# Performance work log

Hardware: AMD Instinct MI355X
Metric: run time of the kernel (lower is better)

The kernel has to match this reference:

```python
import jax, jax.numpy as jnp
import numpy as np

PATCH = 8      # patch_size
NFREQ = 8      # fourie_freq


def _fourier_feats(nH, nW, F, dtype):
    # Per-patch positional Fourier features: sin/cos of normalized patch-center
    # coords at F dyadic frequencies for both axes -> [nH, nW, 4F].
    iy = (jnp.arange(nH, dtype=jnp.float32) + 0.5) / nH
    ix = (jnp.arange(nW, dtype=jnp.float32) + 0.5) / nW
    freqs = (2.0 ** jnp.arange(F, dtype=jnp.float32)) * jnp.pi
    fy = iy[:, None] * freqs[None, :]  # [nH, F]
    fx = ix[:, None] * freqs[None, :]  # [nW, F]
    feats = jnp.concatenate([
        jnp.broadcast_to(jnp.sin(fy)[:, None, :], (nH, nW, F)),
        jnp.broadcast_to(jnp.cos(fy)[:, None, :], (nH, nW, F)),
        jnp.broadcast_to(jnp.sin(fx)[None, :, :], (nH, nW, F)),
        jnp.broadcast_to(jnp.cos(fx)[None, :, :], (nH, nW, F)),
    ], axis=-1)
    return feats.astype(dtype)


def setup_inputs() -> dict:
    key = jax.random.key(0)
    ks = jax.random.split(key, 5)
    B, C, H, W = 16, 64, 128, 128
    E, OC, P, F = 8, 64, PATCH, NFREQ
    GC = C + 4 * F  # gate_channel = 96
    x = jax.random.normal(ks[0], (B, C, H, W), jnp.float32)
    expert_w = jax.random.normal(ks[1], (E, OC, C, 3, 3), jnp.float32) * 0.05
    expert_b = jax.random.normal(ks[2], (E, OC), jnp.float32) * 0.05
    gate_w = jax.random.normal(ks[3], (E, GC * P * P), jnp.float32) * 0.02
    gate_b = jnp.zeros((E,), jnp.float32)
    return {"x": x, "expert_w": expert_w, "expert_b": expert_b,
            "gate_w": gate_w, "gate_b": gate_b}


def reference(x, expert_w, expert_b, gate_w, gate_b):
    B, C, H, W = x.shape
    E, OC = expert_w.shape[0], expert_w.shape[1]
    P, F = PATCH, NFREQ
    nH, nW = H // P, W // P

    # --- gating: per-patch softmax over experts ---
    # patches: [B, nH, nW, C, P, P] (matches nn.Flatten over (C,P,P))
    patches = x.reshape(B, C, nH, P, nW, P).transpose(0, 2, 4, 1, 3, 5)
    feats = _fourier_feats(nH, nW, F, x.dtype)                       # [nH,nW,4F]
    pos = jnp.broadcast_to(feats[None, :, :, :, None, None],
                           (B, nH, nW, 4 * F, P, P))
    gate_in = jnp.concatenate([patches, pos], axis=3).reshape(B, nH, nW, -1)
    logits = jnp.einsum('bhwf,ef->bhwe', gate_in, gate_w) + gate_b
    gate = jax.nn.softmax(logits, axis=-1)                           # [B,nH,nW,E]

    # --- experts: all E convs fused into a single conv, then gated combine ---
    wk = expert_w.reshape(E * OC, C, 3, 3)
    y = jax.lax.conv_general_dilated(
        x, wk, window_strides=(1, 1), padding='SAME',
        dimension_numbers=('NCHW', 'OIHW', 'NCHW'))
    y = y + expert_b.reshape(E * OC)[None, :, None, None]
    y = jax.nn.relu(y).reshape(B, E, OC, H, W)

    # upsample per-patch gates to pixel resolution: [B,E,H,W]
    g = gate.transpose(0, 3, 1, 2)                                   # [B,E,nH,nW]
    g = jnp.repeat(jnp.repeat(g, P, axis=2), P, axis=3)
    out = jnp.einsum('behw,bechw->bchw', g, y)                       # [B,OC,H,W]
    return out
```

## Files before the change

kernel.cpp:

```cpp
#include <hip/hip_runtime.h>

typedef short v8s __attribute__((ext_vector_type(8)));
typedef float v4f __attribute__((ext_vector_type(4)));

#define NCH    64
#define NHH    128
#define NWW    128
#define NOC    64
#define KSTEPS 18

#define COLS 34
#define SLAB_BYTES (6 * COLS * 128)
#define BBUF_OFF   SLAB_BYTES
#define NBUF 3
#define LDSG_OFF   (SLAB_BYTES + NBUF * 8192)
#define SMEM_BYTES (LDSG_OFF + 128)

#define GW_STRIDE 6144

__device__ __forceinline__ unsigned short f2bf(float f) {
  unsigned int u = __float_as_uint(f);
  u += 0x7FFFu + ((u >> 16) & 1u);
  return (unsigned short)(u >> 16);
}

__global__ void pack_b_kernel(const float* __restrict__ ew,
                              unsigned short* __restrict__ bp) {
  int f = blockIdx.x * 256 + threadIdx.x;
  int j = f & 7;
  int t = f >> 3;
  int lane = t & 63;
  t >>= 6;
  int nt = t & 3;
  t >>= 2;
  int e01 = t & 1;
  int gs = t >> 1;
  int sl = gs % KSTEPS;
  int g = gs / KSTEPS;
  int e = g + 4 * e01;
  int k = sl * 32 + (lane >> 4) * 8 + j;
  int n = nt * 16 + (lane & 15);
  int khw = k >> 6;
  int c = k & 63;
  bp[f] = f2bf(ew[((e * NOC + n) * NCH + c) * 9 + khw]);
}

__global__ __launch_bounds__(512) void gate_kernel(
    const float* __restrict__ x,
    const float* __restrict__ gw,
    const float* __restrict__ gb,
    float* __restrict__ gate_out) {
  __shared__ float xs[16][8][132];
  __shared__ float wsum[8][32];
  __shared__ float lg[16][8];

  const int pid = blockIdx.x;
  const int ph = pid & 15;
  const int b = pid >> 4;
  const int tid = threadIdx.x;
  const int e = tid >> 6;
  const int lane = tid & 63;

  if (tid < 256) {
    int e2 = tid >> 5, j = tid & 31;
    const float* p = gw + e2 * GW_STRIDE + 4096 + j * 64;
    float s = 0.f;
#pragma unroll
    for (int g = 0; g < 16; ++g) {
      float4 v = *(const float4*)(p + g * 4);
      s += v.x + v.y + v.z + v.w;
    }
    wsum[e2][j] = s;
  }

  float acc[16];
#pragma unroll
  for (int pw = 0; pw < 16; ++pw) acc[pw] = 0.f;

  const float* xrow = x + ((size_t)(b * NCH) * NHH + ph * 8) * NWW;

  for (int cc = 0; cc < 4; ++cc) {
    __syncthreads();
    for (int i = tid; i < 4096; i += 512) {
      int c = i >> 8;
      int py = (i >> 5) & 7;
      int w4 = i & 31;
      float4 v = *(const float4*)&xrow[(cc * 16 + c) * (NHH * NWW) + py * NWW + w4 * 4];
      *(float4*)&xs[c][py][w4 * 4] = v;
    }
    __syncthreads();
#pragma unroll
    for (int i = 0; i < 4; ++i) {
      int g = lane + 64 * i;
      int pxg = g & 1;
      int py = (g >> 1) & 7;
      int c = g >> 4;
      const float4 wv = *(const float4*)&gw[e * GW_STRIDE + (cc * 16 + c) * 64 + py * 8 + pxg * 4];
      const float* xp = &xs[c][py][pxg * 4];
#pragma unroll
      for (int pw = 0; pw < 16; ++pw) {
        float4 xv = *(const float4*)(xp + pw * 8);
        acc[pw] += xv.x * wv.x + xv.y * wv.y + xv.z * wv.z + xv.w * wv.w;
      }
    }
  }

#pragma unroll
  for (int pw = 0; pw < 16; ++pw) {
    float v = acc[pw];
#pragma unroll
    for (int off = 32; off > 0; off >>= 1) v += __shfl_xor(v, off, 64);
    if (lane == 0) lg[pw][e] = v;
  }
  __syncthreads();

  if (tid < 16) {
    const int pw = tid;
    const float cy = (ph + 0.5f) / 16.0f;
    const float cx = (pw + 0.5f) / 16.0f;
    float l[8];
#pragma unroll
    for (int ee = 0; ee < 8; ++ee) l[ee] = lg[pw][ee] + gb[ee];
    for (int j = 0; j < 32; ++j) {
      float freq = (float)(1 << (j & 7)) * 3.14159265358979323846f;
      float base = (j < 16) ? cy : cx;
      float a = base * freq;
      float v = ((j >> 3) & 1) ? cosf(a) : sinf(a);
#pragma unroll
      for (int ee = 0; ee < 8; ++ee) l[ee] += v * wsum[ee][j];
    }
    float mx = -1e30f;
#pragma unroll
    for (int ee = 0; ee < 8; ++ee) mx = fmaxf(mx, l[ee]);
    float sum = 0.f;
#pragma unroll
    for (int ee = 0; ee < 8; ++ee) { l[ee] = expf(l[ee] - mx); sum += l[ee]; }
    float inv = 1.0f / sum;
#pragma unroll
    for (int ee = 0; ee < 8; ++ee)
      gate_out[(pid * 16 + pw) * 8 + ee] = l[ee] * inv;
  }
}

__device__ __forceinline__ void load_stage(const unsigned short* __restrict__ bp,
                                           char* smem, int gs, int buf,
                                           int wid, int lane) {
  const char* gsrc = (const char*)bp + gs * 8192 + wid * 2048 + lane * 16;
  char* ldst = smem + BBUF_OFF + buf * 8192 + wid * 2048;
  __builtin_amdgcn_global_load_lds(
      (const __attribute__((address_space(1))) void*)gsrc,
      (__attribute__((address_space(3))) void*)ldst, 16, 0, 0);
  __builtin_amdgcn_global_load_lds(
      (const __attribute__((address_space(1))) void*)(gsrc + 1024),
      (__attribute__((address_space(3))) void*)(ldst + 1024), 16, 0, 0);
}

__global__ __launch_bounds__(256, 2) void moe_conv_kernel(
    const float* __restrict__ x,
    const float* __restrict__ eb,
    const unsigned short* __restrict__ bp,
    const float* __restrict__ gate,
    float* __restrict__ out) {
  __shared__ __align__(16) char smem[SMEM_BYTES];
  unsigned short* bbufs = (unsigned short*)(smem + BBUF_OFF);
  float* ldsg = (float*)(smem + LDSG_OFF);

  const int tid = threadIdx.x;
  const int bid = blockIdx.x;
  const int wseg = bid & 3;
  const int hq = (bid >> 2) & 31;
  const int b = bid >> 7;
  const int w0 = wseg * 32;
  const int wid = tid >> 6;
  const int lane = tid & 63;
  const int quad = lane >> 4;
  const int l15 = lane & 15;
  const int rp = wid >> 1;
  const int eh = wid & 1;

  load_stage(bp, smem, 0, 0, wid, lane);

  if (tid < 32) {
    ldsg[tid] = gate[((b * 16 + (hq >> 1)) * 16 + wseg * 4 + (tid >> 3)) * 8 + (tid & 7)];
  }

  const int hbase = hq * 4 - 1;
  const int wbase = w0 - 1;
  for (int flat = tid; flat < 6 * 32 * COLS; flat += 256) {
    int col = flat % COLS;
    int t = flat / COLS;
    int cp = t & 31;
    int r = t >> 5;
    int gh = hbase + r;
    int gw_ = wbase + col;
    float v0 = 0.f, v1 = 0.f;
    if (((unsigned)gh < 128u) && ((unsigned)gw_ < 128u)) {
      const float* px = x + (((b * NCH + cp * 2) * NHH + gh) * NWW + gw_);
      v0 = px[0];
      v1 = px[NHH * NWW];
    }
    unsigned int pk = (unsigned int)f2bf(v0) | ((unsigned int)f2bf(v1) << 16);
    int srow = r * COLS + col;
    int boff = ((cp * 4) + ((srow & 7) << 4)) & 127;
    *(unsigned int*)(smem + srow * 128 + boff) = pk;
  }

  load_stage(bp, smem, 1, 1, wid, lane);
  __syncthreads();

  const v4f vzero = {0.f, 0.f, 0.f, 0.f};
  v4f oacc[4][4];
#pragma unroll
  for (int m = 0; m < 4; ++m)
#pragma unroll
    for (int nt = 0; nt < 4; ++nt) oacc[m][nt] = vzero;

  const int q16 = quad * 16;
  const int s7 = 4 * rp + l15;
  const int rowb0 = ((rp * 2 + 0) * COLS + l15) * 128;
  const int rowb1 = ((rp * 2 + 1) * COLS + l15) * 128;

  for (int g = 0; g < 4; ++g) {
    v4f vacc[4][4];
#pragma unroll
    for (int m = 0; m < 4; ++m)
#pragma unroll
      for (int nt = 0; nt < 4; ++nt) vacc[m][nt] = vzero;

#pragma unroll
    for (int sl = 0; sl < KSTEPS; ++sl) {
      const int gs = g * KSTEPS + sl;
      if (gs > 0) {
        asm volatile("s_waitcnt vmcnt(2)" ::: "memory");
        __builtin_amdgcn_s_barrier();
        __builtin_amdgcn_sched_barrier(0);
      }
      {
        int g2 = gs + 2;
        if (g2 > 71) g2 = 71;
        load_stage(bp, smem, g2, (gs + 2) % 3, wid, lane);
      }

      const unsigned short* bstage = bbufs + (gs % 3) * 4096;
      const int kh = sl / 6;
      const int kw = (sl / 2) % 3;
      const int ch = sl & 1;
      v8s bf[4];
#pragma unroll
      for (int nt = 0; nt < 4; ++nt)
        bf[nt] = *(const v8s*)(bstage + (eh * 4 + nt) * 512 + lane * 8);
      const int kbyte = (kh * COLS + kw) * 128;
      __builtin_amdgcn_s_setprio(1);
#pragma unroll
      for (int r01 = 0; r01 < 2; ++r01) {
        const int rot = ((s7 + 2 * (r01 + kh) + kw) & 7) << 4;
        const int aoff = (q16 + ch * 64 + rot) & 127;
        const int rbase = (r01 ? rowb1 : rowb0) + kbyte + aoff;
#pragma unroll
        for (int ct = 0; ct < 2; ++ct) {
          const v8s a = *(const v8s*)(smem + rbase + ct * 2048);
#pragma unroll
          for (int nt = 0; nt < 4; ++nt)
            vacc[r01 * 2 + ct][nt] =
                __builtin_amdgcn_mfma_f32_16x16x32_bf16(a, bf[nt], vacc[r01 * 2 + ct][nt], 0, 0, 0);
        }
      }
      __builtin_amdgcn_s_setprio(0);
    }

    const int e = g + 4 * eh;
    float bias[4];
#pragma unroll
    for (int nt = 0; nt < 4; ++nt) bias[nt] = eb[e * NOC + nt * 16 + l15];
#pragma unroll
    for (int m = 0; m < 4; ++m) {
      const int ct = m & 1;
      float gv = ldsg[(ct * 2 + (quad >> 1)) * 8 + e];
#pragma unroll
      for (int nt = 0; nt < 4; ++nt)
#pragma unroll
        for (int r = 0; r < 4; ++r) {
          float v = fmaxf(vacc[m][nt][r] + bias[nt], 0.f);
          oacc[m][nt][r] += v * gv;
        }
    }
  }

  __syncthreads();
  float* tbf = (float*)smem;
  if (eh == 0) {
#pragma unroll
    for (int m = 0; m < 4; ++m) {
      const int r01 = m >> 1, ct = m & 1;
#pragma unroll
      for (int nt = 0; nt < 4; ++nt)
        *(v4f*)(tbf + ((rp * 2 + r01) * 64 + nt * 16 + l15) * 36 + ct * 16 + quad * 4) =
            oacc[m][nt];
    }
  }
  __syncthreads();
  if (eh == 1) {
#pragma unroll
    for (int m = 0; m < 4; ++m) {
      const int r01 = m >> 1, ct = m & 1;
#pragma unroll
      for (int nt = 0; nt < 4; ++nt) {
        float* p = tbf + ((rp * 2 + r01) * 64 + nt * 16 + l15) * 36 + ct * 16 + quad * 4;
        v4f t = *(v4f*)p;
        t += oacc[m][nt];
        *(v4f*)p = t;
      }
    }
  }
  __syncthreads();

  const int h = hq * 4 + wid;
  const int l7 = lane & 7;
  const int o8 = lane >> 3;
#pragma unroll
  for (int g4 = 0; g4 < 8; ++g4) {
    const int ocl = g4 * 8 + o8;
    const v4f vv = *(const v4f*)(tbf + (wid * 64 + ocl) * 36 + l7 * 4);
    float* dst = out + ((b * NOC + ocl) * NHH + h) * NWW + w0 + l7 * 4;
    *(v4f*)dst = vv;
  }
}

extern "C" void kernel_launch(void* const* d_in, const int* in_sizes, int n_in,
                              void* d_out, int out_size, void* d_ws, size_t ws_size,
                              hipStream_t stream) {
  const float* x  = (const float*)d_in[0];
  const float* ew = (const float*)d_in[1];
  const float* eb = (const float*)d_in[2];
  const float* gw = (const float*)d_in[3];
  const float* gb = (const float*)d_in[4];
  float* out = (float*)d_out;

  unsigned short* bp = (unsigned short*)d_ws;
  float* gate = (float*)((char*)d_ws + 589824);

  hipLaunchKernelGGL(pack_b_kernel, dim3(1152), dim3(256), 0, stream, ew, bp);
  hipLaunchKernelGGL(gate_kernel, dim3(256), dim3(512), 0, stream, x, gw, gb, gate);
  hipLaunchKernelGGL(moe_conv_kernel, dim3(2048), dim3(256), 0, stream, x, eb, bp, gate, out);
}
```

Baseline: 282.1 us.

## Split waves by output-channel half to drop cross-wave reduction, raise occupancy

Each wave now owns half the output channels for all 8 experts instead of all 64 channels for half the experts. The gated sum then finishes in registers, so the two-pass LDS reduction and its extra barriers go away. The final accumulator shrinks from 16 to 8 v4f, and launch bounds move from 2 to 3 blocks per SIMD to try for more occupancy. The risk is that LDS use (about 58KB per block) or register spilling caps the extra occupancy, and each wave now reads all four B fragments per stage.

```diff
diff --git a/kernel.cpp b/kernel.cpp
--- a/kernel.cpp
+++ b/kernel.cpp
@@ -155,7 +155,7 @@
       (__attribute__((address_space(3))) void*)(ldst + 1024), 16, 0, 0);
 }
 
-__global__ __launch_bounds__(256, 2) void moe_conv_kernel(
+__global__ __launch_bounds__(256, 3) void moe_conv_kernel(
     const float* __restrict__ x,
     const float* __restrict__ eb,
     const unsigned short* __restrict__ bp,
@@ -176,7 +176,7 @@
   const int quad = lane >> 4;
   const int l15 = lane & 15;
   const int rp = wid >> 1;
-  const int eh = wid & 1;
+  const int och = wid & 1;
 
   load_stage(bp, smem, 0, 0, wid, lane);
 
@@ -209,11 +209,12 @@
   __syncthreads();
 
   const v4f vzero = {0.f, 0.f, 0.f, 0.f};
-  v4f oacc[4][4];
-#pragma unroll
-  for (int m = 0; m < 4; ++m)
-#pragma unroll
-    for (int nt = 0; nt < 4; ++nt) oacc[m][nt] = vzero;
+  v4f oacc[4][2];
+#pragma unroll
+  for (int m = 0; m < 4; ++m) {
+    oacc[m][0] = vzero;
+    oacc[m][1] = vzero;
+  }
 
   const int q16 = quad * 16;
   const int s7 = 4 * rp + l15;
@@ -221,11 +222,14 @@
   const int rowb1 = ((rp * 2 + 1) * COLS + l15) * 128;
 
   for (int g = 0; g < 4; ++g) {
-    v4f vacc[4][4];
+    v4f vacc[4][2][2];
 #pragma unroll
     for (int m = 0; m < 4; ++m)
 #pragma unroll
-      for (int nt = 0; nt < 4; ++nt) vacc[m][nt] = vzero;
+      for (int e01 = 0; e01 < 2; ++e01) {
+        vacc[m][e01][0] = vzero;
+        vacc[m][e01][1] = vzero;
+      }
 
 #pragma unroll
     for (int sl = 0; sl < KSTEPS; ++sl) {
@@ -245,10 +249,12 @@
       const int kh = sl / 6;
       const int kw = (sl / 2) % 3;
       const int ch = sl & 1;
-      v8s bf[4];
-#pragma unroll
-      for (int nt = 0; nt < 4; ++nt)
-        bf[nt] = *(const v8s*)(bstage + (eh * 4 + nt) * 512 + lane * 8);
+      v8s bf[2][2];
+#pragma unroll
+      for (int e01 = 0; e01 < 2; ++e01)
+#pragma unroll
+        for (int j = 0; j < 2; ++j)
+          bf[e01][j] = *(const v8s*)(bstage + (e01 * 4 + och * 2 + j) * 512 + lane * 8);
       const int kbyte = (kh * COLS + kw) * 128;
       __builtin_amdgcn_s_setprio(1);
 #pragma unroll
@@ -259,70 +265,61 @@
 #pragma unroll
         for (int ct = 0; ct < 2; ++ct) {
           const v8s a = *(const v8s*)(smem + rbase + ct * 2048);
-#pragma unroll
-          for (int nt = 0; nt < 4; ++nt)
-            vacc[r01 * 2 + ct][nt] =
-                __builtin_amdgcn_mfma_f32_16x16x32_bf16(a, bf[nt], vacc[r01 * 2 + ct][nt], 0, 0, 0);
+          const int m = r01 * 2 + ct;
+#pragma unroll
+          for (int e01 = 0; e01 < 2; ++e01)
+#pragma unroll
+            for (int j = 0; j < 2; ++j)
+              vacc[m][e01][j] =
+                  __builtin_amdgcn_mfma_f32_16x16x32_bf16(a, bf[e01][j], vacc[m][e01][j], 0, 0, 0);
         }
       }
       __builtin_amdgcn_s_setprio(0);
     }
 
-    const int e = g + 4 * eh;
-    float bias[4];
-#pragma unroll
-    for (int nt = 0; nt < 4; ++nt) bias[nt] = eb[e * NOC + nt * 16 + l15];
-#pragma unroll
-    for (int m = 0; m < 4; ++m) {
-      const int ct = m & 1;
-      float gv = ldsg[(ct * 2 + (quad >> 1)) * 8 + e];
-#pragma unroll
-      for (int nt = 0; nt < 4; ++nt)
-#pragma unroll
-        for (int r = 0; r < 4; ++r) {
-          float v = fmaxf(vacc[m][nt][r] + bias[nt], 0.f);
-          oacc[m][nt][r] += v * gv;
-        }
+#pragma unroll
+    for (int e01 = 0; e01 < 2; ++e01) {
+      const int e = g + 4 * e01;
+      float bias[2];
+      bias[0] = eb[e * NOC + (och * 2 + 0) * 16 + l15];
+      bias[1] = eb[e * NOC + (och * 2 + 1) * 16 + l15];
+#pragma unroll
+      for (int m = 0; m < 4; ++m) {
+        const int ct = m & 1;
+        float gv = ldsg[(ct * 2 + (quad >> 1)) * 8 + e];
+#pragma unroll
+        for (int j = 0; j < 2; ++j)
+#pragma unroll
+          for (int r = 0; r < 4; ++r) {
+            float v = fmaxf(vacc[m][e01][j][r] + bias[j], 0.f);
+            oacc[m][j][r] += v * gv;
+          }
+      }
     }
   }
 
   __syncthreads();
-  float* tbf = (float*)smem;
-  if (eh == 0) {
-#pragma unroll
-    for (int m = 0; m < 4; ++m) {
-      const int r01 = m >> 1, ct = m & 1;
-#pragma unroll
-      for (int nt = 0; nt < 4; ++nt)
-        *(v4f*)(tbf + ((rp * 2 + r01) * 64 + nt * 16 + l15) * 36 + ct * 16 + quad * 4) =
-            oacc[m][nt];
-    }
-  }
-  __syncthreads();
-  if (eh == 1) {
-#pragma unroll
-    for (int m = 0; m < 4; ++m) {
-      const int r01 = m >> 1, ct = m & 1;
-#pragma unroll
-      for (int nt = 0; nt < 4; ++nt) {
-        float* p = tbf + ((rp * 2 + r01) * 64 + nt * 16 + l15) * 36 + ct * 16 + quad * 4;
-        v4f t = *(v4f*)p;
-        t += oacc[m][nt];
-        *(v4f*)p = t;
-      }
-    }
-  }
-  __syncthreads();
-
-  const int h = hq * 4 + wid;
+  float* tb = (float*)smem + wid * 2304;
+#pragma unroll
+  for (int m = 0; m < 4; ++m) {
+    const int r01 = m >> 1, ct = m & 1;
+#pragma unroll
+    for (int j = 0; j < 2; ++j)
+      *(v4f*)(tb + (r01 * 32 + j * 16 + l15) * 36 + ct * 16 + quad * 4) = oacc[m][j];
+  }
+
   const int l7 = lane & 7;
   const int o8 = lane >> 3;
 #pragma unroll
-  for (int g4 = 0; g4 < 8; ++g4) {
-    const int ocl = g4 * 8 + o8;
-    const v4f vv = *(const v4f*)(tbf + (wid * 64 + ocl) * 36 + l7 * 4);
-    float* dst = out + ((b * NOC + ocl) * NHH + h) * NWW + w0 + l7 * 4;
-    *(v4f*)dst = vv;
+  for (int r01 = 0; r01 < 2; ++r01) {
+    const int h = hq * 4 + rp * 2 + r01;
+#pragma unroll
+    for (int g4 = 0; g4 < 4; ++g4) {
+      const int ocl = g4 * 8 + o8;
+      const v4f vv = *(const v4f*)(tb + (r01 * 32 + ocl) * 36 + l7 * 4);
+      float* dst = out + ((b * NOC + och * 32 + ocl) * NHH + h) * NWW + w0 + l7 * 4;
+      *(v4f*)dst = vv;
+    }
   }
 }
 
```

Result: slower. 303.5 us (+7.6%).
